# Kernel optimization log

Measured on AMD Instinct MI355X. Metric: run time of the kernel, lower is better.

## Reference

```python
import jax, jax.numpy as jnp
import numpy as np

N_NODES = 100000
N_EDGES = 1600000
IN_CH = 256
OUT_CH = 128


def setup_inputs() -> dict:
    key = jax.random.key(0)
    k1, k2, k3, k4, k5, k6 = jax.random.split(key, 6)
    x = jax.random.normal(k1, (N_NODES, IN_CH), dtype=jnp.float32)
    edge_src = jax.random.randint(k2, (N_EDGES,), 0, N_NODES, dtype=jnp.int32)
    edge_dst = jax.random.randint(k3, (N_EDGES,), 0, N_NODES, dtype=jnp.int32)
    edge_weight = jax.random.uniform(k4, (N_EDGES,), dtype=jnp.float32)
    # Linear params (torch nn.Linear: y = x @ W.T + b)
    W = jax.random.normal(k5, (OUT_CH, IN_CH), dtype=jnp.float32) * (1.0 / np.sqrt(IN_CH))
    b = jax.random.normal(k6, (OUT_CH,), dtype=jnp.float32) * 0.01
    return {"x": x, "edge_src": edge_src, "edge_dst": edge_dst,
            "edge_weight": edge_weight, "W": W, "b": b}


def reference(x, edge_src, edge_dst, edge_weight, W, b):
    # Linear projection: [N, in] -> [N, out]
    h = x @ W.T + b
    # spmm sum aggregation: out[d] = sum_{e: dst(e)=d} w_e * h[src(e)]
    msgs = h[edge_src] * edge_weight[:, None]  # [E, out]
    out = jax.ops.segment_sum(msgs, edge_dst, num_segments=N_NODES)
    return out
```

## Files before the change

### kernel.cpp

```cpp
#include <hip/hip_runtime.h>
#include <hip/hip_bf16.h>

#define IN_CH 256
#define OUT_CH 128
#define BKT_SHIFT 7
#define BKT_SIZE 128
#define BSUB 64
#define MAXNB 1024
#define K3_CHUNK 8192
#define MAXBLK 256
#define BATCH 3072
#define CAPP 4096

using bf16x8 = __attribute__((ext_vector_type(8))) __bf16;
using f32x16 = __attribute__((ext_vector_type(16))) float;
using f32x4  = __attribute__((ext_vector_type(4))) float;
using f32x2  = __attribute__((ext_vector_type(2))) float;

__device__ __forceinline__ unsigned int f2bf(float f) {
    union { float f; unsigned u; } v; v.f = f;
    unsigned r = v.u + 0x7fffu + ((v.u >> 16) & 1u);
    return r >> 16;
}
__device__ __forceinline__ float bf2f(unsigned short u) {
    union { unsigned u; float f; } v; v.u = ((unsigned)u) << 16;
    return v.f;
}

__global__ void __launch_bounds__(256) prep_w(const float* __restrict__ W,
                                              unsigned short* __restrict__ Wfrag) {
    const int flat = blockIdx.x * 256 + threadIdx.x;
    const int l = flat & 63;
    const int ks = (flat >> 6) & 15;
    const int c = flat >> 10;
    const int row = c * 32 + (l & 31);
    const int col0 = ks * 16 + 8 * (l >> 5);
    const float* src = W + (size_t)row * IN_CH + col0;
    uint4 o;
    o.x = f2bf(src[0]) | (f2bf(src[1]) << 16);
    o.y = f2bf(src[2]) | (f2bf(src[3]) << 16);
    o.z = f2bf(src[4]) | (f2bf(src[5]) << 16);
    o.w = f2bf(src[6]) | (f2bf(src[7]) << 16);
    *reinterpret_cast<uint4*>(Wfrag + (size_t)flat * 8) = o;
}

__global__ void __launch_bounds__(512) linear_mfma(
    const float* __restrict__ x, const unsigned short* __restrict__ Wfrag,
    const float* __restrict__ b, unsigned short* __restrict__ h, int n_nodes) {
    __shared__ uint4 wlds[4096];
    const int tid = threadIdx.x;
    const int w = tid >> 6, l = tid & 63;
    const int l31 = l & 31, lh = l >> 5;
    const int node0 = blockIdx.x * 256 + w * 32;

    {
        const uint4* wfg = reinterpret_cast<const uint4*>(Wfrag);
#pragma unroll
        for (int j = 0; j < 8; ++j) wlds[j * 512 + tid] = wfg[j * 512 + tid];
    }
    __syncthreads();

    int arow = node0 + l31;
    if (arow > n_nodes - 1) arow = n_nodes - 1;
    const float* xrow = x + (size_t)arow * IN_CH + 8 * lh;

    f32x16 acc0 = {}, acc1 = {}, acc2 = {}, acc3 = {};

#pragma unroll 4
    for (int ks = 0; ks < 16; ++ks) {
        float4 a0 = *reinterpret_cast<const float4*>(xrow + ks * 16);
        float4 a1 = *reinterpret_cast<const float4*>(xrow + ks * 16 + 4);
        bf16x8 af;
        af[0] = (__bf16)a0.x; af[1] = (__bf16)a0.y;
        af[2] = (__bf16)a0.z; af[3] = (__bf16)a0.w;
        af[4] = (__bf16)a1.x; af[5] = (__bf16)a1.y;
        af[6] = (__bf16)a1.z; af[7] = (__bf16)a1.w;

        uint4 bw0 = wlds[(0 * 16 + ks) * 64 + l];
        uint4 bw1 = wlds[(1 * 16 + ks) * 64 + l];
        uint4 bw2 = wlds[(2 * 16 + ks) * 64 + l];
        uint4 bw3 = wlds[(3 * 16 + ks) * 64 + l];

        acc0 = __builtin_amdgcn_mfma_f32_32x32x16_bf16(af, __builtin_bit_cast(bf16x8, bw0), acc0, 0, 0, 0);
        acc1 = __builtin_amdgcn_mfma_f32_32x32x16_bf16(af, __builtin_bit_cast(bf16x8, bw1), acc1, 0, 0, 0);
        acc2 = __builtin_amdgcn_mfma_f32_32x32x16_bf16(af, __builtin_bit_cast(bf16x8, bw2), acc2, 0, 0, 0);
        acc3 = __builtin_amdgcn_mfma_f32_32x32x16_bf16(af, __builtin_bit_cast(bf16x8, bw3), acc3, 0, 0, 0);
    }

    const float bias0 = b[0 + l31], bias1 = b[32 + l31], bias2 = b[64 + l31], bias3 = b[96 + l31];
#pragma unroll
    for (int reg = 0; reg < 16; ++reg) {
        const int r = (reg & 3) + 8 * (reg >> 2) + 4 * lh;
        const int node = node0 + r;
        if (node < n_nodes) {
            unsigned short* hp = h + (size_t)node * OUT_CH;
            __bf16 t0 = (__bf16)(acc0[reg] + bias0);
            __bf16 t1 = (__bf16)(acc1[reg] + bias1);
            __bf16 t2 = (__bf16)(acc2[reg] + bias2);
            __bf16 t3 = (__bf16)(acc3[reg] + bias3);
            hp[0 + l31]  = __builtin_bit_cast(unsigned short, t0);
            hp[32 + l31] = __builtin_bit_cast(unsigned short, t1);
            hp[64 + l31] = __builtin_bit_cast(unsigned short, t2);
            hp[96 + l31] = __builtin_bit_cast(unsigned short, t3);
        }
    }
}

__global__ void __launch_bounds__(512) k1_hist(
    const int* __restrict__ edge_dst, int* __restrict__ bh, int n_edges, int nb) {
    __shared__ int hist[MAXNB];
    const int t = threadIdx.x;
    const int blk = blockIdx.x;
    for (int i = t; i < MAXNB; i += 512) hist[i] = 0;
    __syncthreads();
    const int base = blk * K3_CHUNK;
#pragma unroll
    for (int j = 0; j < K3_CHUNK / 512; ++j) {
        int e = base + j * 512 + t;
        if (e < n_edges) atomicAdd(&hist[edge_dst[e] >> BKT_SHIFT], 1);
    }
    __syncthreads();
    for (int i = t; i < nb; i += 512) bh[i * MAXBLK + blk] = hist[i];
}

__global__ void __launch_bounds__(256) k2a_scan_cols(
    const int* __restrict__ bh, int* __restrict__ offs, int* __restrict__ total,
    int nblk) {
    __shared__ int sd[256];
    const int t = threadIdx.x;
    const int bkt = blockIdx.x;
    int val = (t < nblk) ? bh[bkt * MAXBLK + t] : 0;
    sd[t] = val;
    __syncthreads();
    for (int s = 1; s < 256; s <<= 1) {
        int y = (t >= s) ? sd[t - s] : 0;
        __syncthreads();
        sd[t] += y;
        __syncthreads();
    }
    offs[bkt * MAXBLK + t] = sd[t] - val;
    if (t == 255) total[bkt] = sd[255];
}

__global__ void __launch_bounds__(256) k2b_scan_base(
    const int* __restrict__ total, int* __restrict__ base, int nb) {
    __shared__ int sd[256];
    const int t = threadIdx.x;
    int v[4];
    int loc = 0;
#pragma unroll
    for (int k = 0; k < 4; ++k) {
        int idx = t * 4 + k;
        v[k] = (idx < nb) ? total[idx] : 0;
        loc += v[k];
    }
    sd[t] = loc;
    __syncthreads();
    for (int s = 1; s < 256; s <<= 1) {
        int y = (t >= s) ? sd[t - s] : 0;
        __syncthreads();
        sd[t] += y;
        __syncthreads();
    }
    int run = sd[t] - loc;
#pragma unroll
    for (int k = 0; k < 4; ++k) {
        int idx = t * 4 + k;
        if (idx < nb) base[idx] = run;
        run += v[k];
    }
    if (t == 255) base[nb] = sd[255];
}

__global__ void __launch_bounds__(512) k3_bin(
    const int* __restrict__ edge_src, const int* __restrict__ edge_dst,
    const float* __restrict__ edge_weight,
    const int* __restrict__ offs, const int* __restrict__ base,
    unsigned long long* __restrict__ records, int n_edges, int nb) {
    __shared__ unsigned long long staged[K3_CHUNK];
    __shared__ int hist[MAXNB];
    __shared__ int cur[MAXNB];
    __shared__ int gbase[MAXNB];
    __shared__ int sd[512];

    const int t = threadIdx.x;
    const int blk = blockIdx.x;
    const int ebase = blk * K3_CHUNK;
    const int count = min(K3_CHUNK, n_edges - ebase);

    for (int i = t; i < MAXNB; i += 512) hist[i] = 0;
    __syncthreads();
#pragma unroll
    for (int j = 0; j < K3_CHUNK / 512; ++j) {
        int e = ebase + j * 512 + t;
        if (e < n_edges) atomicAdd(&hist[edge_dst[e] >> BKT_SHIFT], 1);
    }
    __syncthreads();
    int h0 = hist[2 * t], h1 = hist[2 * t + 1];
    int loc = h0 + h1;
    sd[t] = loc;
    __syncthreads();
    for (int s = 1; s < 512; s <<= 1) {
        int y = (t >= s) ? sd[t - s] : 0;
        __syncthreads();
        sd[t] += y;
        __syncthreads();
    }
    int excl = sd[t] - loc;
    cur[2 * t] = excl;
    cur[2 * t + 1] = excl + h0;
    if (2 * t < nb)     gbase[2 * t]     = base[2 * t]     + offs[(2 * t) * MAXBLK + blk]     - excl;
    if (2 * t + 1 < nb) gbase[2 * t + 1] = base[2 * t + 1] + offs[(2 * t + 1) * MAXBLK + blk] - (excl + h0);
    __syncthreads();
#pragma unroll
    for (int j = 0; j < K3_CHUNK / 512; ++j) {
        int e = ebase + j * 512 + t;
        if (e < n_edges) {
            int d = edge_dst[e];
            int bkt = d >> BKT_SHIFT;
            unsigned int wbits = f2bf(edge_weight[e]);
            unsigned long long rec = ((unsigned long long)wbits << 48) |
                                     ((unsigned long long)bkt << 24) |
                                     ((unsigned long long)(d & (BKT_SIZE - 1)) << 17) |
                                     (unsigned int)edge_src[e];
            int pos = atomicAdd(&cur[bkt], 1);
            staged[pos] = rec;
        }
    }
    __syncthreads();
    for (int i = t; i < count; i += 512) {
        unsigned long long r = staged[i];
        int bkt = (int)((r >> 24) & 1023u);
        records[gbase[bkt] + i] = r;
    }
}

__global__ void __launch_bounds__(512) k4_agg(
    const unsigned short* __restrict__ h, const unsigned long long* __restrict__ records,
    const int* __restrict__ base, float* __restrict__ out, int n_nodes) {
    __shared__ unsigned long long sorted[CAPP];
    __shared__ int hist[BSUB];
    __shared__ int cur[BSUB];
    __shared__ int pstart[BSUB];
    __shared__ int sd[BSUB];
    __shared__ int ptot;

    const int t = threadIdx.x;
    const int bkt = blockIdx.x >> 1;
    const int sub = blockIdx.x & 1;
    const int w = t >> 6, lane = t & 63;
    const int rbeg = base[bkt], rend = base[bkt + 1];

    float acc[8][2];
#pragma unroll
    for (int d = 0; d < 8; ++d) { acc[d][0] = 0.f; acc[d][1] = 0.f; }

    for (int b0 = rbeg; b0 < rend; b0 += BATCH) {
        const int cnt = min(BATCH, rend - b0);
        __syncthreads();
        unsigned long long r[6];
        int keep[6];
#pragma unroll
        for (int j = 0; j < 6; ++j) {
            const int o = j * 512 + t;
            r[j] = (o < cnt) ? records[b0 + o] : 0ull;
            const int dl7 = (int)((unsigned)(r[j] >> 17) & 127u);
            keep[j] = (o < cnt) && ((dl7 >> 6) == sub);
        }
        if (t < BSUB) hist[t] = 0;
        __syncthreads();
#pragma unroll
        for (int j = 0; j < 6; ++j)
            if (keep[j]) atomicAdd(&hist[(unsigned)(r[j] >> 17) & 63u], 1);
        __syncthreads();
        if (t < BSUB) sd[t] = (hist[t] + 7) & ~7;
        __syncthreads();
        for (int s = 1; s < BSUB; s <<= 1) {
            int y = 0;
            if (t < BSUB && t >= s) y = sd[t - s];
            __syncthreads();
            if (t < BSUB) sd[t] += y;
            __syncthreads();
        }
        if (t < BSUB) {
            const int e = sd[t] - ((hist[t] + 7) & ~7);
            pstart[t] = e;
            cur[t] = e;
        }
        if (t == BSUB - 1) ptot = sd[BSUB - 1];
        __syncthreads();
        const int pt = ptot;
        for (int i = t; i < pt; i += 512) sorted[i] = 0ull;
        __syncthreads();
#pragma unroll
        for (int j = 0; j < 6; ++j) {
            if (keep[j]) {
                const int dl = (int)((unsigned)(r[j] >> 17) & 63u);
                const int pos = atomicAdd(&cur[dl], 1);
                sorted[pos] = r[j];
            }
        }
        __syncthreads();
#pragma unroll
        for (int d = 0; d < 8; ++d) {
            const int dl = w * 8 + d;
            const int s0 = pstart[dl];
            const int s1 = s0 + hist[dl];
            float a0 = 0.f, a1 = 0.f;
            for (int i = s0; i < s1; i += 8) {
                unsigned int hv[8];
                float wt[8];
#pragma unroll
                for (int j = 0; j < 8; ++j) {
                    const unsigned long long rr = sorted[i + j];
                    const unsigned lo = __builtin_amdgcn_readfirstlane((unsigned)rr);
                    const unsigned hi = __builtin_amdgcn_readfirstlane((unsigned)(rr >> 32));
                    wt[j] = __builtin_bit_cast(float, hi & 0xFFFF0000u);
                    const unsigned* hp = reinterpret_cast<const unsigned*>(
                        h + (size_t)(lo & 0x1FFFFu) * OUT_CH);
                    hv[j] = hp[lane];
                }
#pragma unroll
                for (int j = 0; j < 8; ++j) {
                    a0 += wt[j] * __builtin_bit_cast(float, hv[j] << 16);
                    a1 += wt[j] * __builtin_bit_cast(float, hv[j] & 0xFFFF0000u);
                }
            }
            acc[d][0] += a0;
            acc[d][1] += a1;
        }
    }

#pragma unroll
    for (int d = 0; d < 8; ++d) {
        const int node = bkt * BKT_SIZE + sub * BSUB + w * 8 + d;
        if (node < n_nodes) {
            f32x2 v = {acc[d][0], acc[d][1]};
            __builtin_nontemporal_store(
                v, reinterpret_cast<f32x2*>(out + (size_t)node * OUT_CH + 2 * lane));
        }
    }
}

extern "C" void kernel_launch(void* const* d_in, const int* in_sizes, int n_in,
                              void* d_out, int out_size, void* d_ws, size_t ws_size,
                              hipStream_t stream) {
    const float* x           = (const float*)d_in[0];
    const int*   edge_src    = (const int*)d_in[1];
    const int*   edge_dst    = (const int*)d_in[2];
    const float* edge_weight = (const float*)d_in[3];
    const float* W           = (const float*)d_in[4];
    const float* b           = (const float*)d_in[5];
    float* out = (float*)d_out;

    const int n_nodes = in_sizes[0] / IN_CH;
    const int n_edges = in_sizes[1];
    const int nb = (n_nodes + BKT_SIZE - 1) / BKT_SIZE;
    const int nblk = (n_edges + K3_CHUNK - 1) / K3_CHUNK;

    unsigned long long* records = (unsigned long long*)d_ws;
    unsigned short* h  = (unsigned short*)(records + n_edges);
    int* bh    = (int*)(h + (size_t)n_nodes * OUT_CH);
    int* offs  = bh + MAXNB * MAXBLK;
    int* total = offs + MAXNB * MAXBLK;
    int* base  = total + MAXNB;
    unsigned short* Wfrag = (unsigned short*)(base + MAXNB + 2);

    prep_w<<<16, 256, 0, stream>>>(W, Wfrag);
    linear_mfma<<<(n_nodes + 255) / 256, 512, 0, stream>>>(x, Wfrag, b, h, n_nodes);
    k1_hist<<<nblk, 512, 0, stream>>>(edge_dst, bh, n_edges, nb);
    k2a_scan_cols<<<nb, 256, 0, stream>>>(bh, offs, total, nblk);
    k2b_scan_base<<<1, 256, 0, stream>>>(total, base, nb);
    k3_bin<<<nblk, 512, 0, stream>>>(edge_src, edge_dst, edge_weight,
                                     offs, base, records, n_edges, nb);
    k4_agg<<<nb * 2, 512, 0, stream>>>(h, records, base, out, n_nodes);
}
```

Measured before the change: 130.6 us.

## Bin edges by 64-node destination bins, fold W prep into histogram kernel

```diff
diff --git a/kernel.cpp b/kernel.cpp
--- a/kernel.cpp
+++ b/kernel.cpp
@@ -3,14 +3,13 @@
 
 #define IN_CH 256
 #define OUT_CH 128
-#define BKT_SHIFT 7
-#define BKT_SIZE 128
-#define BSUB 64
-#define MAXNB 1024
-#define K3_CHUNK 8192
-#define MAXBLK 256
-#define BATCH 3072
-#define CAPP 4096
+#define BIN_SHIFT 6
+#define BIN_SIZE 64
+#define MAXNB2 2048
+#define CHUNK3 4096
+#define NBLK_MAX 512
+#define K4BATCH 1536
+#define K4CAP 2048
 
 using bf16x8 = __attribute__((ext_vector_type(8))) __bf16;
 using f32x16 = __attribute__((ext_vector_type(16))) float;
@@ -22,26 +21,89 @@
     unsigned r = v.u + 0x7fffu + ((v.u >> 16) & 1u);
     return r >> 16;
 }
-__device__ __forceinline__ float bf2f(unsigned short u) {
-    union { unsigned u; float f; } v; v.u = ((unsigned)u) << 16;
-    return v.f;
-}
-
-__global__ void __launch_bounds__(256) prep_w(const float* __restrict__ W,
-                                              unsigned short* __restrict__ Wfrag) {
-    const int flat = blockIdx.x * 256 + threadIdx.x;
-    const int l = flat & 63;
-    const int ks = (flat >> 6) & 15;
-    const int c = flat >> 10;
-    const int row = c * 32 + (l & 31);
-    const int col0 = ks * 16 + 8 * (l >> 5);
-    const float* src = W + (size_t)row * IN_CH + col0;
-    uint4 o;
-    o.x = f2bf(src[0]) | (f2bf(src[1]) << 16);
-    o.y = f2bf(src[2]) | (f2bf(src[3]) << 16);
-    o.z = f2bf(src[4]) | (f2bf(src[5]) << 16);
-    o.w = f2bf(src[6]) | (f2bf(src[7]) << 16);
-    *reinterpret_cast<uint4*>(Wfrag + (size_t)flat * 8) = o;
+
+__global__ void __launch_bounds__(512) k1_hist(
+    const float* __restrict__ W, unsigned short* __restrict__ Wfrag,
+    const int* __restrict__ edge_dst, unsigned short* __restrict__ bh,
+    int n_edges, int nb2) {
+    const int t = threadIdx.x;
+    if (blockIdx.x < 8) {
+        const int flat = blockIdx.x * 512 + t;
+        const int l = flat & 63;
+        const int ks = (flat >> 6) & 15;
+        const int c = flat >> 10;
+        const int row = c * 32 + (l & 31);
+        const int col0 = ks * 16 + 8 * (l >> 5);
+        const float* src = W + (size_t)row * IN_CH + col0;
+        uint4 o;
+        o.x = f2bf(src[0]) | (f2bf(src[1]) << 16);
+        o.y = f2bf(src[2]) | (f2bf(src[3]) << 16);
+        o.z = f2bf(src[4]) | (f2bf(src[5]) << 16);
+        o.w = f2bf(src[6]) | (f2bf(src[7]) << 16);
+        *reinterpret_cast<uint4*>(Wfrag + (size_t)flat * 8) = o;
+        return;
+    }
+    __shared__ int hist[MAXNB2];
+    const int blk = blockIdx.x - 8;
+    for (int i = t; i < MAXNB2; i += 512) hist[i] = 0;
+    __syncthreads();
+    const int base = blk * CHUNK3;
+#pragma unroll
+    for (int j = 0; j < CHUNK3 / 512; ++j) {
+        int e = base + j * 512 + t;
+        if (e < n_edges) atomicAdd(&hist[edge_dst[e] >> BIN_SHIFT], 1);
+    }
+    __syncthreads();
+    for (int i = t; i < nb2; i += 512) bh[(size_t)i * NBLK_MAX + blk] = (unsigned short)hist[i];
+}
+
+__global__ void __launch_bounds__(512) k2a_scan_cols(
+    const unsigned short* __restrict__ bh, unsigned short* __restrict__ offs,
+    int* __restrict__ total, int nblk) {
+    __shared__ int sd[512];
+    const int t = threadIdx.x;
+    const int bin = blockIdx.x;
+    int val = (t < nblk) ? (int)bh[(size_t)bin * NBLK_MAX + t] : 0;
+    sd[t] = val;
+    __syncthreads();
+    for (int s = 1; s < 512; s <<= 1) {
+        int y = (t >= s) ? sd[t - s] : 0;
+        __syncthreads();
+        sd[t] += y;
+        __syncthreads();
+    }
+    offs[(size_t)bin * NBLK_MAX + t] = (unsigned short)(sd[t] - val);
+    if (t == 511) total[bin] = sd[511];
+}
+
+__global__ void __launch_bounds__(512) k2b_scan_base(
+    const int* __restrict__ total, int* __restrict__ base, int nb2) {
+    __shared__ int sd[512];
+    const int t = threadIdx.x;
+    int v[4];
+    int loc = 0;
+#pragma unroll
+    for (int k = 0; k < 4; ++k) {
+        int idx = t * 4 + k;
+        v[k] = (idx < nb2) ? total[idx] : 0;
+        loc += v[k];
+    }
+    sd[t] = loc;
+    __syncthreads();
+    for (int s = 1; s < 512; s <<= 1) {
+        int y = (t >= s) ? sd[t - s] : 0;
+        __syncthreads();
+        sd[t] += y;
+        __syncthreads();
+    }
+    int run = sd[t] - loc;
+#pragma unroll
+    for (int k = 0; k < 4; ++k) {
+        int idx = t * 4 + k;
+        if (idx < nb2) base[idx] = run;
+        run += v[k];
+    }
+    if (t == 511) base[nb2] = sd[511];
 }
 
 __global__ void __launch_bounds__(512) linear_mfma(
@@ -106,98 +168,32 @@
     }
 }
 
-__global__ void __launch_bounds__(512) k1_hist(
-    const int* __restrict__ edge_dst, int* __restrict__ bh, int n_edges, int nb) {
-    __shared__ int hist[MAXNB];
-    const int t = threadIdx.x;
-    const int blk = blockIdx.x;
-    for (int i = t; i < MAXNB; i += 512) hist[i] = 0;
-    __syncthreads();
-    const int base = blk * K3_CHUNK;
-#pragma unroll
-    for (int j = 0; j < K3_CHUNK / 512; ++j) {
-        int e = base + j * 512 + t;
-        if (e < n_edges) atomicAdd(&hist[edge_dst[e] >> BKT_SHIFT], 1);
-    }
-    __syncthreads();
-    for (int i = t; i < nb; i += 512) bh[i * MAXBLK + blk] = hist[i];
-}
-
-__global__ void __launch_bounds__(256) k2a_scan_cols(
-    const int* __restrict__ bh, int* __restrict__ offs, int* __restrict__ total,
-    int nblk) {
-    __shared__ int sd[256];
-    const int t = threadIdx.x;
-    const int bkt = blockIdx.x;
-    int val = (t < nblk) ? bh[bkt * MAXBLK + t] : 0;
-    sd[t] = val;
-    __syncthreads();
-    for (int s = 1; s < 256; s <<= 1) {
-        int y = (t >= s) ? sd[t - s] : 0;
-        __syncthreads();
-        sd[t] += y;
-        __syncthreads();
-    }
-    offs[bkt * MAXBLK + t] = sd[t] - val;
-    if (t == 255) total[bkt] = sd[255];
-}
-
-__global__ void __launch_bounds__(256) k2b_scan_base(
-    const int* __restrict__ total, int* __restrict__ base, int nb) {
-    __shared__ int sd[256];
-    const int t = threadIdx.x;
-    int v[4];
-    int loc = 0;
-#pragma unroll
-    for (int k = 0; k < 4; ++k) {
-        int idx = t * 4 + k;
-        v[k] = (idx < nb) ? total[idx] : 0;
-        loc += v[k];
-    }
-    sd[t] = loc;
-    __syncthreads();
-    for (int s = 1; s < 256; s <<= 1) {
-        int y = (t >= s) ? sd[t - s] : 0;
-        __syncthreads();
-        sd[t] += y;
-        __syncthreads();
-    }
-    int run = sd[t] - loc;
-#pragma unroll
-    for (int k = 0; k < 4; ++k) {
-        int idx = t * 4 + k;
-        if (idx < nb) base[idx] = run;
-        run += v[k];
-    }
-    if (t == 255) base[nb] = sd[255];
-}
-
 __global__ void __launch_bounds__(512) k3_bin(
     const int* __restrict__ edge_src, const int* __restrict__ edge_dst,
     const float* __restrict__ edge_weight,
-    const int* __restrict__ offs, const int* __restrict__ base,
-    unsigned long long* __restrict__ records, int n_edges, int nb) {
-    __shared__ unsigned long long staged[K3_CHUNK];
-    __shared__ int hist[MAXNB];
-    __shared__ int cur[MAXNB];
-    __shared__ int gbase[MAXNB];
+    const unsigned short* __restrict__ offs, const int* __restrict__ base,
+    unsigned long long* __restrict__ records, int n_edges, int nb2) {
+    __shared__ unsigned long long staged[CHUNK3];
+    __shared__ int hist[MAXNB2];
+    __shared__ int cur[MAXNB2];
+    __shared__ int gbase[MAXNB2];
     __shared__ int sd[512];
 
     const int t = threadIdx.x;
     const int blk = blockIdx.x;
-    const int ebase = blk * K3_CHUNK;
-    const int count = min(K3_CHUNK, n_edges - ebase);
-
-    for (int i = t; i < MAXNB; i += 512) hist[i] = 0;
-    __syncthreads();
-#pragma unroll
-    for (int j = 0; j < K3_CHUNK / 512; ++j) {
+    const int ebase = blk * CHUNK3;
+    const int count = min(CHUNK3, n_edges - ebase);
+
+    for (int i = t; i < MAXNB2; i += 512) hist[i] = 0;
+    __syncthreads();
+#pragma unroll
+    for (int j = 0; j < CHUNK3 / 512; ++j) {
         int e = ebase + j * 512 + t;
-        if (e < n_edges) atomicAdd(&hist[edge_dst[e] >> BKT_SHIFT], 1);
-    }
-    __syncthreads();
-    int h0 = hist[2 * t], h1 = hist[2 * t + 1];
-    int loc = h0 + h1;
+        if (e < n_edges) atomicAdd(&hist[edge_dst[e] >> BIN_SHIFT], 1);
+    }
+    __syncthreads();
+    int h0 = hist[4 * t], h1 = hist[4 * t + 1], h2 = hist[4 * t + 2], h3 = hist[4 * t + 3];
+    int loc = h0 + h1 + h2 + h3;
     sd[t] = loc;
     __syncthreads();
     for (int s = 1; s < 512; s <<= 1) {
@@ -207,103 +203,103 @@
         __syncthreads();
     }
     int excl = sd[t] - loc;
-    cur[2 * t] = excl;
-    cur[2 * t + 1] = excl + h0;
-    if (2 * t < nb)     gbase[2 * t]     = base[2 * t]     + offs[(2 * t) * MAXBLK + blk]     - excl;
-    if (2 * t + 1 < nb) gbase[2 * t + 1] = base[2 * t + 1] + offs[(2 * t + 1) * MAXBLK + blk] - (excl + h0);
-    __syncthreads();
-#pragma unroll
-    for (int j = 0; j < K3_CHUNK / 512; ++j) {
+    {
+        int run = excl;
+        cur[4 * t] = run; run += h0;
+        cur[4 * t + 1] = run; run += h1;
+        cur[4 * t + 2] = run; run += h2;
+        cur[4 * t + 3] = run;
+    }
+    {
+        int run = excl;
+#pragma unroll
+        for (int k = 0; k < 4; ++k) {
+            int bin = 4 * t + k;
+            if (bin < nb2)
+                gbase[bin] = base[bin] + (int)offs[(size_t)bin * NBLK_MAX + blk] - run;
+            run += (k == 0 ? h0 : k == 1 ? h1 : k == 2 ? h2 : h3);
+        }
+    }
+    __syncthreads();
+#pragma unroll
+    for (int j = 0; j < CHUNK3 / 512; ++j) {
         int e = ebase + j * 512 + t;
         if (e < n_edges) {
             int d = edge_dst[e];
-            int bkt = d >> BKT_SHIFT;
+            int bin = d >> BIN_SHIFT;
             unsigned int wbits = f2bf(edge_weight[e]);
             unsigned long long rec = ((unsigned long long)wbits << 48) |
-                                     ((unsigned long long)bkt << 24) |
-                                     ((unsigned long long)(d & (BKT_SIZE - 1)) << 17) |
+                                     ((unsigned long long)bin << 24) |
+                                     ((unsigned long long)(d & (BIN_SIZE - 1)) << 17) |
                                      (unsigned int)edge_src[e];
-            int pos = atomicAdd(&cur[bkt], 1);
+            int pos = atomicAdd(&cur[bin], 1);
             staged[pos] = rec;
         }
     }
     __syncthreads();
     for (int i = t; i < count; i += 512) {
         unsigned long long r = staged[i];
-        int bkt = (int)((r >> 24) & 1023u);
-        records[gbase[bkt] + i] = r;
-    }
-}
-
-__global__ void __launch_bounds__(512) k4_agg(
+        int bin = (int)((r >> 24) & 4095u);
+        records[gbase[bin] + i] = r;
+    }
+}
+
+__global__ void __launch_bounds__(256) k4_agg(
     const unsigned short* __restrict__ h, const unsigned long long* __restrict__ records,
     const int* __restrict__ base, float* __restrict__ out, int n_nodes) {
-    __shared__ unsigned long long sorted[CAPP];
-    __shared__ int hist[BSUB];
-    __shared__ int cur[BSUB];
-    __shared__ int pstart[BSUB];
-    __shared__ int sd[BSUB];
+    __shared__ unsigned long long sorted[K4CAP];
+    __shared__ int hist[BIN_SIZE];
+    __shared__ int cur[BIN_SIZE];
+    __shared__ int pstart[BIN_SIZE];
+    __shared__ int sd[BIN_SIZE];
     __shared__ int ptot;
 
     const int t = threadIdx.x;
-    const int bkt = blockIdx.x >> 1;
-    const int sub = blockIdx.x & 1;
+    const int bin = blockIdx.x;
     const int w = t >> 6, lane = t & 63;
-    const int rbeg = base[bkt], rend = base[bkt + 1];
-
-    float acc[8][2];
-#pragma unroll
-    for (int d = 0; d < 8; ++d) { acc[d][0] = 0.f; acc[d][1] = 0.f; }
-
-    for (int b0 = rbeg; b0 < rend; b0 += BATCH) {
-        const int cnt = min(BATCH, rend - b0);
-        __syncthreads();
-        unsigned long long r[6];
-        int keep[6];
-#pragma unroll
-        for (int j = 0; j < 6; ++j) {
-            const int o = j * 512 + t;
-            r[j] = (o < cnt) ? records[b0 + o] : 0ull;
-            const int dl7 = (int)((unsigned)(r[j] >> 17) & 127u);
-            keep[j] = (o < cnt) && ((dl7 >> 6) == sub);
-        }
-        if (t < BSUB) hist[t] = 0;
-        __syncthreads();
-#pragma unroll
-        for (int j = 0; j < 6; ++j)
-            if (keep[j]) atomicAdd(&hist[(unsigned)(r[j] >> 17) & 63u], 1);
-        __syncthreads();
-        if (t < BSUB) sd[t] = (hist[t] + 7) & ~7;
-        __syncthreads();
-        for (int s = 1; s < BSUB; s <<= 1) {
+    const int rbeg = base[bin], rend = base[bin + 1];
+
+    float acc[16][2];
+#pragma unroll
+    for (int d = 0; d < 16; ++d) { acc[d][0] = 0.f; acc[d][1] = 0.f; }
+
+    for (int b0 = rbeg; b0 < rend; b0 += K4BATCH) {
+        const int cnt = min(K4BATCH, rend - b0);
+        __syncthreads();
+        if (t < BIN_SIZE) hist[t] = 0;
+        __syncthreads();
+        for (int i = t; i < cnt; i += 256)
+            atomicAdd(&hist[(unsigned)(records[b0 + i] >> 17) & 63u], 1);
+        __syncthreads();
+        if (t < BIN_SIZE) sd[t] = (hist[t] + 7) & ~7;
+        __syncthreads();
+        for (int s = 1; s < BIN_SIZE; s <<= 1) {
             int y = 0;
-            if (t < BSUB && t >= s) y = sd[t - s];
+            if (t < BIN_SIZE && t >= s) y = sd[t - s];
             __syncthreads();
-            if (t < BSUB) sd[t] += y;
+            if (t < BIN_SIZE) sd[t] += y;
             __syncthreads();
         }
-        if (t < BSUB) {
+        if (t < BIN_SIZE) {
             const int e = sd[t] - ((hist[t] + 7) & ~7);
             pstart[t] = e;
             cur[t] = e;
         }
-        if (t == BSUB - 1) ptot = sd[BSUB - 1];
+        if (t == BIN_SIZE - 1) ptot = sd[BIN_SIZE - 1];
         __syncthreads();
         const int pt = ptot;
-        for (int i = t; i < pt; i += 512) sorted[i] = 0ull;
-        __syncthreads();
-#pragma unroll
-        for (int j = 0; j < 6; ++j) {
-            if (keep[j]) {
-                const int dl = (int)((unsigned)(r[j] >> 17) & 63u);
-                const int pos = atomicAdd(&cur[dl], 1);
-                sorted[pos] = r[j];
-            }
-        }
-        __syncthreads();
-#pragma unroll
-        for (int d = 0; d < 8; ++d) {
-            const int dl = w * 8 + d;
+        for (int i = t; i < pt; i += 256) sorted[i] = 0ull;
+        __syncthreads();
+        for (int i = t; i < cnt; i += 256) {
+            const unsigned long long r = records[b0 + i];
+            const int dl = (int)((unsigned)(r >> 17) & 63u);
+            const int pos = atomicAdd(&cur[dl], 1);
+            sorted[pos] = r;
+        }
+        __syncthreads();
+#pragma unroll
+        for (int d = 0; d < 16; ++d) {
+            const int dl = w * 16 + d;
             const int s0 = pstart[dl];
             const int s1 = s0 + hist[dl];
             float a0 = 0.f, a1 = 0.f;
@@ -332,8 +328,8 @@
     }
 
 #pragma unroll
-    for (int d = 0; d < 8; ++d) {
-        const int node = bkt * BKT_SIZE + sub * BSUB + w * 8 + d;
+    for (int d = 0; d < 16; ++d) {
+        const int node = bin * BIN_SIZE + w * 16 + d;
         if (node < n_nodes) {
             f32x2 v = {acc[d][0], acc[d][1]};
             __builtin_nontemporal_store(
@@ -355,23 +351,22 @@
 
     const int n_nodes = in_sizes[0] / IN_CH;
     const int n_edges = in_sizes[1];
-    const int nb = (n_nodes + BKT_SIZE - 1) / BKT_SIZE;
-    const int nblk = (n_edges + K3_CHUNK - 1) / K3_CHUNK;
+    const int nb2 = (n_nodes + BIN_SIZE - 1) / BIN_SIZE;
+    const int nblk = (n_edges + CHUNK3 - 1) / CHUNK3;
 
     unsigned long long* records = (unsigned long long*)d_ws;
-    unsigned short* h  = (unsigned short*)(records + n_edges);
-    int* bh    = (int*)(h + (size_t)n_nodes * OUT_CH);
-    int* offs  = bh + MAXNB * MAXBLK;
-    int* total = offs + MAXNB * MAXBLK;
-    int* base  = total + MAXNB;
-    unsigned short* Wfrag = (unsigned short*)(base + MAXNB + 2);
-
-    prep_w<<<16, 256, 0, stream>>>(W, Wfrag);
+    unsigned short* h     = (unsigned short*)(records + n_edges);
+    unsigned short* bh    = (unsigned short*)(h + (size_t)n_nodes * OUT_CH);
+    unsigned short* offs  = bh + (size_t)MAXNB2 * NBLK_MAX;
+    int* total = (int*)(offs + (size_t)MAXNB2 * NBLK_MAX);
+    int* base  = total + MAXNB2;
+    unsigned short* Wfrag = (unsigned short*)(base + MAXNB2 + 2);
+
+    k1_hist<<<8 + nblk, 512, 0, stream>>>(W, Wfrag, edge_dst, bh, n_edges, nb2);
+    k2a_scan_cols<<<nb2, 512, 0, stream>>>(bh, offs, total, nblk);
+    k2b_scan_base<<<1, 512, 0, stream>>>(total, base, nb2);
     linear_mfma<<<(n_nodes + 255) / 256, 512, 0, stream>>>(x, Wfrag, b, h, n_nodes);
-    k1_hist<<<nblk, 512, 0, stream>>>(edge_dst, bh, n_edges, nb);
-    k2a_scan_cols<<<nb, 256, 0, stream>>>(bh, offs, total, nblk);
-    k2b_scan_base<<<1, 256, 0, stream>>>(total, base, nb);
     k3_bin<<<nblk, 512, 0, stream>>>(edge_src, edge_dst, edge_weight,
-                                     offs, base, records, n_edges, nb);
-    k4_agg<<<nb * 2, 512, 0, stream>>>(h, records, base, out, n_nodes);
-}
+                                     offs, base, records, n_edges, nb2);
+    k4_agg<<<nb2, 256, 0, stream>>>(h, records, base, out, n_nodes);
+}
```

Measured after the change: 135.6 us. 3.8% more time.
